# Optimization experiments

Measured on AMD Instinct MI355X. Metric: run time of the kernel, lower is better.

Reference implementation:

```python
import jax, jax.numpy as jnp
import numpy as np

L, H, W, C = 5, 32, 128, 256
HEADS, DH = 8, 32
NUM_TYPES, NUM_REL = 2, 4
INNER = HEADS * DH  # 256
LN_EPS = 1e-5


def setup_inputs() -> dict:
    key = jax.random.key(0)
    ks = jax.random.split(key, 16)
    s = 0.05
    x = jax.random.normal(ks[0], (L, H, W, C), jnp.float32)
    mask = jax.random.randint(ks[1], (H, W, 1, L), 0, 2).astype(jnp.int32)
    types = jax.random.randint(ks[2], (L,), 0, NUM_TYPES)
    # prior_encoding carries the node type in channel 2 (constant across H,W)
    prior_encoding = jnp.zeros((L, H, W, 3), jnp.float32)
    prior_encoding = prior_encoding.at[:, :, :, 2].set(
        jnp.broadcast_to(types[:, None, None].astype(jnp.float32), (L, H, W)))
    return {
        'x': x,
        'mask': mask,
        'prior_encoding': prior_encoding,
        'ln_gamma': jnp.ones((C,), jnp.float32),
        'ln_beta': jnp.zeros((C,), jnp.float32),
        'q_weight': jax.random.normal(ks[3], (NUM_TYPES, INNER, C), jnp.float32) * s,
        'q_bias': jnp.zeros((NUM_TYPES, INNER), jnp.float32),
        'k_weight': jax.random.normal(ks[4], (NUM_TYPES, INNER, C), jnp.float32) * s,
        'k_bias': jnp.zeros((NUM_TYPES, INNER), jnp.float32),
        'v_weight': jax.random.normal(ks[5], (NUM_TYPES, INNER, C), jnp.float32) * s,
        'v_bias': jnp.zeros((NUM_TYPES, INNER), jnp.float32),
        'a_weight': jax.random.normal(ks[6], (NUM_TYPES, C, INNER), jnp.float32) * s,
        'a_bias': jnp.zeros((NUM_TYPES, C), jnp.float32),
        'relation_att': jax.random.normal(ks[7], (NUM_REL, HEADS, DH, DH), jnp.float32) * s,
        'relation_msg': jax.random.normal(ks[8], (NUM_REL, HEADS, DH, DH), jnp.float32) * s,
    }


def reference(x, mask, prior_encoding, ln_gamma, ln_beta,
              q_weight, q_bias, k_weight, k_bias, v_weight, v_bias,
              a_weight, a_bias, relation_att, relation_msg):
    # --- prenorm (LayerNorm over last dim), x: (L,H,W,C) ---
    mu = jnp.mean(x, axis=-1, keepdims=True)
    var = jnp.mean(jnp.square(x - mu), axis=-1, keepdims=True)
    xn = (x - mu) * jax.lax.rsqrt(var + LN_EPS) * ln_gamma + ln_beta

    xh = jnp.transpose(xn, (1, 2, 0, 3))  # (H,W,L,C)
    types = prior_encoding[:, 0, 0, 2].astype(jnp.int32)
    types = jnp.clip(types, 0, None)  # (L,)
    n_types = q_weight.shape[0]
    heads, dh = relation_att.shape[1], relation_att.shape[2]
    Hh, Ww, Ll = xh.shape[0], xh.shape[1], xh.shape[2]

    def type_linear(w, b):  # per-token typed projection
        return jnp.einsum('hwlc,lic->hwli', xh, w[types]) + b[types]

    def to_heads(t):  # (H,W,L,inner) -> (m,H,W,L,dh)
        return jnp.transpose(t.reshape(Hh, Ww, Ll, heads, dh), (3, 0, 1, 2, 4))

    q = to_heads(type_linear(q_weight, q_bias))
    k = to_heads(type_linear(k_weight, k_bias))
    v = to_heads(type_linear(v_weight, v_bias))

    # per-edge relation matrices: rel_idx (L,L)
    rel_idx = types[:, None] * n_types + types[None, :]
    w_att = jnp.transpose(relation_att[rel_idx], (2, 0, 1, 3, 4))  # (m,L,L,dh,dh)
    w_msg = jnp.transpose(relation_msg[rel_idx], (2, 0, 1, 3, 4))  # (m,L,L,dh,dh)

    scale = jnp.asarray(dh, jnp.float32) ** -0.5
    # att_map = (q @ w_att) @ k^T, per (head, h, w, i, j)
    att = jnp.einsum('mhwip,mijpq,mhwjq->mhwij', q, w_att, k) * scale
    att = jnp.where(mask[None] == 0, jnp.float32(-1e9), att)  # mask: (1,H,W,1,L)
    att = jax.nn.softmax(att, axis=-1)

    # out = att @ (w_msg @ v)
    out = jnp.einsum('mhwij,mijpc,mhwjp->mhwic', att, w_msg, v)  # (m,H,W,L,dh)
    out = jnp.transpose(out, (1, 2, 3, 0, 4)).reshape(Hh, Ww, Ll, heads * dh)

    # typed output projection back to C
    out = jnp.einsum('hwli,lci->hwlc', out, a_weight[types]) + a_bias[types]
    return jnp.transpose(out, (2, 0, 1, 3))  # (L,H,W,C)
```

## Files before the change

kernel.cpp:

```cpp
#include <hip/hip_runtime.h>
#include <math.h>

#define LL 5
#define HH 32
#define WW 128
#define CC 256
#define HEADS 8
#define DHH 32
#define HW (HH*WW)
#define NTOK (LL*HW)
#define LN_EPS 1e-5f

typedef short bf16x8 __attribute__((ext_vector_type(8)));
typedef float f32x4 __attribute__((ext_vector_type(4)));
typedef unsigned short u16x8 __attribute__((ext_vector_type(8)));

__device__ __forceinline__ int clamp01(int t) { return t < 0 ? 0 : (t > 1 ? 1 : t); }

__device__ __forceinline__ unsigned short f2b(float f) {
    union { float f; unsigned u; } v; v.f = f;
    unsigned r = v.u + 0x7FFFu + ((v.u >> 16) & 1u);
    return (unsigned short)(r >> 16);
}
__device__ __forceinline__ float b2f(unsigned short u) {
    union { unsigned u; float f; } v; v.u = ((unsigned)u) << 16; return v.f;
}

__device__ __forceinline__ size_t frag_off(int row, int col) {
    return ((size_t)((row >> 4) * 8 + (col >> 5)) << 9)
         + (((col & 31) >> 3) << 7) + ((row & 15) << 3) + (col & 7);
}

__global__ __launch_bounds__(256) void setup_kernel(
        const float* __restrict__ x, const float* __restrict__ g, const float* __restrict__ b,
        unsigned short* __restrict__ xn,
        const float* __restrict__ qw, const float* __restrict__ aw,
        unsigned short* __restrict__ qwb, unsigned short* __restrict__ awb,
        const float* __restrict__ relA, const float* __restrict__ relM,
        const float* __restrict__ kw, const float* __restrict__ vw,
        const float* __restrict__ kb, const float* __restrict__ vb,
        unsigned short* __restrict__ wattb, unsigned short* __restrict__ wmsgb,
        float* __restrict__ batt, float* __restrict__ bmsg) {
    __shared__ float Bl[32][256];
    int blk = blockIdx.x;
    int wave = threadIdx.x >> 6, lane = threadIdx.x & 63;
    if (blk < 1280) {
        float4 gv = *(const float4*)(g + lane * 4);
        float4 bv = *(const float4*)(b + lane * 4);
        #pragma unroll
        for (int rr = 0; rr < 4; ++rr) {
            int row = blk * 16 + wave * 4 + rr;
            const float4 xv = *(const float4*)(x + (size_t)row * CC + lane * 4);
            float s1 = xv.x + xv.y + xv.z + xv.w;
            float s2 = xv.x * xv.x + xv.y * xv.y + xv.z * xv.z + xv.w * xv.w;
            #pragma unroll
            for (int off = 32; off; off >>= 1) {
                s1 += __shfl_xor(s1, off, 64);
                s2 += __shfl_xor(s2, off, 64);
            }
            float mu = s1 * (1.0f / CC);
            float inv = rsqrtf(s2 * (1.0f / CC) - mu * mu + LN_EPS);
            ushort4 o;
            o.x = f2b((xv.x - mu) * inv * gv.x + bv.x);
            o.y = f2b((xv.y - mu) * inv * gv.y + bv.y);
            o.z = f2b((xv.z - mu) * inv * gv.z + bv.z);
            o.w = f2b((xv.w - mu) * inv * gv.w + bv.w);
            *(ushort4*)(xn + frag_off(row, lane << 2)) = o;
        }
    } else if (blk < 1408) {
        int task = (blk - 1280) * 4 + wave;
        int mtx = task >> 8, rem = task & 255;
        int t = rem >> 7, panel = (rem >> 3) & 15, kk = rem & 7;
        const float* S = (mtx ? aw : qw) + (size_t)t * 65536
                       + (size_t)(panel * 16 + (lane & 15)) * 256 + kk * 32 + (lane >> 4) * 8;
        float4 f0 = *(const float4*)S;
        float4 f1 = *(const float4*)(S + 4);
        u16x8 o;
        o[0] = f2b(f0.x); o[1] = f2b(f0.y); o[2] = f2b(f0.z); o[3] = f2b(f0.w);
        o[4] = f2b(f1.x); o[5] = f2b(f1.y); o[6] = f2b(f1.z); o[7] = f2b(f1.w);
        unsigned short* D = (mtx ? awb : qwb) + (size_t)t * 65536
                          + (((size_t)(panel * 8 + kk)) << 9) + (lane << 3);
        *(u16x8*)D = o;
    } else {
        int fb = blk - 1408;
        int r = fb & 3, m = (fb >> 2) & 7, which = fb >> 5;
        int tsel = r & 1;
        const float* S  = (which ? relM : relA) + ((size_t)r * 8 + m) * 1024;
        const float* Bg = (which ? vw : kw) + (size_t)tsel * 65536 + (size_t)m * 32 * 256;
        const float* bv = (which ? vb : kb) + tsel * 256 + m * 32;
        unsigned short* Wf = (which ? wmsgb : wattb) + (size_t)r * 65536;
        float* bo = (which ? bmsg : batt) + r * 256 + m * 32;

        for (int i = threadIdx.x; i < 32 * 256; i += 256)
            Bl[i >> 8][i & 255] = Bg[(size_t)(i >> 8) * 256 + (i & 255)];
        __syncthreads();

        int a  = threadIdx.x >> 3;
        int c0 = (threadIdx.x & 7) * 4;
        float srow[32];
        #pragma unroll
        for (int bq = 0; bq < 32; ++bq)
            srow[bq] = which ? S[bq * 32 + a] : S[a * 32 + bq];
        float acc[8][4] = {{0.f}};
        #pragma unroll
        for (int bq = 0; bq < 32; ++bq) {
            float s = srow[bq];
            #pragma unroll
            for (int cc = 0; cc < 8; ++cc) {
                float4 bb = *(const float4*)&Bl[bq][c0 + cc * 32];
                acc[cc][0] += s * bb.x; acc[cc][1] += s * bb.y;
                acc[cc][2] += s * bb.z; acc[cc][3] += s * bb.w;
            }
        }
        int colpanel = m * 2 + (a >> 4);
        int jr = a & 15;
        #pragma unroll
        for (int cc = 0; cc < 8; ++cc) {
            ushort4 w4;
            w4.x = f2b(acc[cc][0]); w4.y = f2b(acc[cc][1]);
            w4.z = f2b(acc[cc][2]); w4.w = f2b(acc[cc][3]);
            *(ushort4*)(Wf + (((size_t)(colpanel * 8 + cc)) << 9)
                           + ((c0 >> 3) << 7) + (jr << 3) + (c0 & 7)) = w4;
        }
        if (threadIdx.x < 32) {
            int p = threadIdx.x;
            float s = 0.f;
            #pragma unroll
            for (int bq = 0; bq < 32; ++bq)
                s += (which ? S[bq * 32 + p] : S[p * 32 + bq]) * bv[bq];
            bo[p] = s;
        }
    }
}

__global__ __launch_bounds__(256) void gemm_qkv(const short* __restrict__ X,
        const short* __restrict__ qwb, const short* __restrict__ wattb,
        const short* __restrict__ wmsgb,
        const float* __restrict__ qb, const float* __restrict__ batt,
        const float* __restrict__ bmsg,
        const float* __restrict__ prior, unsigned short* __restrict__ OutBase) {
    __shared__ float R[4][16][68];
    int blkrow = blockIdx.x * 32;
    int s = blockIdx.y;
    int l = blkrow >> 12;
    int t = clamp01((int)prior[(size_t)l * HW * 3 + 2]);

    const short* Wp; const float* Bp;
    if (s == 0)      { Wp = qwb   + (size_t)t * 65536;                          Bp = qb   + t * 256; }
    else if (s <= 2) { int i2 = (s - 1) * 2 + t; Wp = wattb + (size_t)i2 * 65536; Bp = batt + i2 * 256; }
    else             { int i2 = (s - 3) * 2 + t; Wp = wmsgb + (size_t)i2 * 65536; Bp = bmsg + i2 * 256; }
    unsigned short* Out = OutBase + (size_t)s * NTOK * 256;

    int wave = threadIdx.x >> 6, lane = threadIdx.x & 63;
    int lr = lane & 15;
    const short* Xf = X + ((size_t)blockIdx.x << 13);

    f32x4 acc[2][4];
    #pragma unroll
    for (int mr = 0; mr < 2; ++mr)
        #pragma unroll
        for (int nr = 0; nr < 4; ++nr) acc[mr][nr] = (f32x4){0.f, 0.f, 0.f, 0.f};

    #pragma unroll
    for (int kk = 0; kk < 8; ++kk) {
        bf16x8 af[2], bf[4];
        #pragma unroll
        for (int mr = 0; mr < 2; ++mr)
            af[mr] = *(const bf16x8*)(Xf + (((size_t)(mr * 8 + kk)) << 9) + (lane << 3));
        #pragma unroll
        for (int nr = 0; nr < 4; ++nr)
            bf[nr] = *(const bf16x8*)(Wp + (((size_t)((wave * 4 + nr) * 8 + kk)) << 9) + (lane << 3));
        #pragma unroll
        for (int mr = 0; mr < 2; ++mr)
            #pragma unroll
            for (int nr = 0; nr < 4; ++nr)
                acc[mr][nr] = __builtin_amdgcn_mfma_f32_16x16x32_bf16(af[mr], bf[nr], acc[mr][nr], 0, 0, 0);
    }

    float bias[4];
    #pragma unroll
    for (int nr = 0; nr < 4; ++nr) bias[nr] = Bp[wave * 64 + nr * 16 + lr];

    int q = lane >> 4;
    int c8 = lane & 7;
    #pragma unroll
    for (int mr = 0; mr < 2; ++mr) {
        #pragma unroll
        for (int nr = 0; nr < 4; ++nr)
            #pragma unroll
            for (int rr = 0; rr < 4; ++rr)
                R[wave][q * 4 + rr][nr * 16 + lr] = acc[mr][nr][rr] + bias[nr];
        #pragma unroll
        for (int p = 0; p < 2; ++p) {
            int r = (lane >> 3) + p * 8;
            float4 v0 = *(const float4*)&R[wave][r][c8 * 8];
            float4 v1 = *(const float4*)&R[wave][r][c8 * 8 + 4];
            u16x8 w;
            w[0] = f2b(v0.x); w[1] = f2b(v0.y); w[2] = f2b(v0.z); w[3] = f2b(v0.w);
            w[4] = f2b(v1.x); w[5] = f2b(v1.y); w[6] = f2b(v1.z); w[7] = f2b(v1.w);
            *(u16x8*)(Out + (size_t)(blkrow + mr * 16 + r) * 256 + wave * 64 + c8 * 8) = w;
        }
        __builtin_amdgcn_wave_barrier();
    }
}

__global__ __launch_bounds__(256) void attn_tl(
        const unsigned short* __restrict__ QKV,
        const int* __restrict__ mask, const float* __restrict__ prior,
        unsigned short* __restrict__ attb) {
    const size_t TSTR = (size_t)NTOK * 256;
    int gid = blockIdx.x * 256 + threadIdx.x;
    int m  = gid & 7;
    int hw = (gid >> 3) & (HW - 1);
    int i  = gid >> 15;
    int t  = clamp01((int)prior[(size_t)i * HW * 3 + 2]);

    const unsigned short* Qp = QKV + (size_t)(i * HW + hw) * 256 + m * 32;
    const unsigned short* Kb = QKV + (1 + t) * TSTR + (size_t)hw * 256 + m * 32;
    const unsigned short* Vb = QKV + (3 + t) * TSTR + (size_t)hw * 256 + m * 32;

    float qf[32];
    #pragma unroll
    for (int c = 0; c < 4; ++c) {
        bf16x8 qv = *(const bf16x8*)(Qp + c * 8);
        #pragma unroll
        for (int e = 0; e < 8; ++e) qf[c * 8 + e] = b2f((unsigned short)qv[e]);
    }

    const float scale = 0.17677669529663687f;
    float s[LL];
    #pragma unroll
    for (int j = 0; j < LL; ++j) {
        const unsigned short* Kp = Kb + (size_t)j * HW * 256;
        float acc = 0.f;
        #pragma unroll
        for (int c = 0; c < 4; ++c) {
            bf16x8 kv = *(const bf16x8*)(Kp + c * 8);
            #pragma unroll
            for (int e = 0; e < 8; ++e)
                acc = fmaf(qf[c * 8 + e], b2f((unsigned short)kv[e]), acc);
        }
        int mk = mask[hw * LL + j];
        s[j] = mk ? acc * scale : -1e9f;
    }

    float mx = fmaxf(fmaxf(fmaxf(s[0], s[1]), fmaxf(s[2], s[3])), s[4]);
    float e5[LL], sum = 0.f;
    #pragma unroll
    for (int j = 0; j < LL; ++j) { e5[j] = __expf(s[j] - mx); sum += e5[j]; }
    float inv = 1.f / sum;

    float o[32];
    #pragma unroll
    for (int c = 0; c < 32; ++c) o[c] = 0.f;
    #pragma unroll
    for (int j = 0; j < LL; ++j) {
        const unsigned short* Vp = Vb + (size_t)j * HW * 256;
        float ej = e5[j];
        #pragma unroll
        for (int c = 0; c < 4; ++c) {
            bf16x8 vv = *(const bf16x8*)(Vp + c * 8);
            #pragma unroll
            for (int e = 0; e < 8; ++e)
                o[c * 8 + e] = fmaf(ej, b2f((unsigned short)vv[e]), o[c * 8 + e]);
        }
    }

    int row = i * HW + hw;
    size_t base = (((size_t)((row >> 4) * 8 + m)) << 9) + ((row & 15) << 3);
    #pragma unroll
    for (int c8 = 0; c8 < 4; ++c8) {
        u16x8 w;
        #pragma unroll
        for (int e = 0; e < 8; ++e) w[e] = f2b(o[c8 * 8 + e] * inv);
        *(u16x8*)(attb + base + c8 * 128) = w;
    }
}

__global__ __launch_bounds__(256) void gemm_a(const short* __restrict__ X,
        const short* __restrict__ W, const float* __restrict__ Bias,
        const float* __restrict__ prior, float* __restrict__ Out) {
    int blkrow = blockIdx.x * 64;
    int l = blkrow >> 12;
    int t = clamp01((int)prior[(size_t)l * HW * 3 + 2]);
    const short* Wp = W + (size_t)t * 65536;
    const float* Bp = Bias + (size_t)t * 256;

    int wave = threadIdx.x >> 6, lane = threadIdx.x & 63;
    int lr = lane & 15;
    const short* Xf = X + (((size_t)blockIdx.x * 4) << 12);

    f32x4 acc[4][4];
    #pragma unroll
    for (int mr = 0; mr < 4; ++mr)
        #pragma unroll
        for (int nr = 0; nr < 4; ++nr) acc[mr][nr] = (f32x4){0.f, 0.f, 0.f, 0.f};

    #pragma unroll
    for (int kk = 0; kk < 8; ++kk) {
        bf16x8 af[4], bf[4];
        #pragma unroll
        for (int mr = 0; mr < 4; ++mr)
            af[mr] = *(const bf16x8*)(Xf + (((size_t)(mr * 8 + kk)) << 9) + (lane << 3));
        #pragma unroll
        for (int nr = 0; nr < 4; ++nr)
            bf[nr] = *(const bf16x8*)(Wp + (((size_t)((wave * 4 + nr) * 8 + kk)) << 9) + (lane << 3));
        #pragma unroll
        for (int mr = 0; mr < 4; ++mr)
            #pragma unroll
            for (int nr = 0; nr < 4; ++nr)
                acc[mr][nr] = __builtin_amdgcn_mfma_f32_16x16x32_bf16(af[mr], bf[nr], acc[mr][nr], 0, 0, 0);
    }

    #pragma unroll
    for (int nr = 0; nr < 4; ++nr) {
        int col = wave * 64 + nr * 16 + lr;
        float bias = Bp[col];
        #pragma unroll
        for (int mr = 0; mr < 4; ++mr) {
            #pragma unroll
            for (int rr = 0; rr < 4; ++rr) {
                int row = blkrow + mr * 16 + (lane >> 4) * 4 + rr;
                Out[(size_t)row * 256 + col] = acc[mr][nr][rr] + bias;
            }
        }
    }
}

extern "C" void kernel_launch(void* const* d_in, const int* in_sizes, int n_in,
                              void* d_out, int out_size, void* d_ws, size_t ws_size,
                              hipStream_t stream) {
    (void)in_sizes; (void)n_in; (void)out_size; (void)ws_size;
    const float* x     = (const float*)d_in[0];
    const int*   mask  = (const int*)d_in[1];
    const float* prior = (const float*)d_in[2];
    const float* ln_g  = (const float*)d_in[3];
    const float* ln_b  = (const float*)d_in[4];
    const float* qw    = (const float*)d_in[5];
    const float* qb    = (const float*)d_in[6];
    const float* kw    = (const float*)d_in[7];
    const float* kb    = (const float*)d_in[8];
    const float* vw    = (const float*)d_in[9];
    const float* vb    = (const float*)d_in[10];
    const float* aw    = (const float*)d_in[11];
    const float* ab    = (const float*)d_in[12];
    const float* relA  = (const float*)d_in[13];
    const float* relM  = (const float*)d_in[14];
    float* out = (float*)d_out;

    char* ws = (char*)d_ws;
    const size_t TOKB = (size_t)NTOK * 256 * 2;
    unsigned short* xnb  = (unsigned short*)(ws);
    unsigned short* Qb   = (unsigned short*)(ws + TOKB);
    unsigned short* attb = (unsigned short*)(ws + 6 * TOKB);
    char* wsp = ws + 7 * TOKB;
    unsigned short* qwb   = (unsigned short*)(wsp);            wsp += 131072 * 2;
    unsigned short* awb   = (unsigned short*)(wsp);            wsp += 131072 * 2;
    unsigned short* wattb = (unsigned short*)(wsp);            wsp += 4 * 65536 * 2;
    unsigned short* wmsgb = (unsigned short*)(wsp);            wsp += 4 * 65536 * 2;
    float* batt = (float*)(wsp);                               wsp += 4 * 256 * 4;
    float* bmsg = (float*)(wsp);

    setup_kernel<<<1472, 256, 0, stream>>>(x, ln_g, ln_b, xnb, qw, aw, qwb, awb,
                                           relA, relM, kw, vw, kb, vb,
                                           wattb, wmsgb, batt, bmsg);

    gemm_qkv<<<dim3(NTOK / 32, 5), 256, 0, stream>>>((const short*)xnb,
            (const short*)qwb, (const short*)wattb, (const short*)wmsgb,
            qb, batt, bmsg, prior, Qb);

    attn_tl<<<(LL * HEADS * HW) / 256, 256, 0, stream>>>(Qb, mask, prior, attb);

    gemm_a<<<NTOK / 64, 256, 0, stream>>>((const short*)attb, (const short*)awb, ab, prior, out);
}
```

Before: 69.82 us.

## Fuse attention and output projection into one kernel via LDS staging

Merges the per-token attention kernel with the typed output-projection GEMM. Each block computes attention for 32 tokens × 8 heads, writes the bf16 results into shared memory in the MFMA panel layout, then runs the projection GEMM straight from LDS. This removes the global round trip of the attention buffer and one kernel launch. In exchange, the GEMM tile shrinks from 64 to 32 rows, so projection weights are reloaded twice as often and each block's GEMM waits behind a barrier.

```diff
diff --git a/kernel.cpp b/kernel.cpp
--- a/kernel.cpp
+++ b/kernel.cpp
@@ -204,109 +204,105 @@
     }
 }
 
-__global__ __launch_bounds__(256) void attn_tl(
-        const unsigned short* __restrict__ QKV,
-        const int* __restrict__ mask, const float* __restrict__ prior,
-        unsigned short* __restrict__ attb) {
+__global__ __launch_bounds__(256) void attn_proj(
+        const unsigned short* __restrict__ QKV, const short* __restrict__ awb,
+        const float* __restrict__ ab, const int* __restrict__ mask,
+        const float* __restrict__ prior, float* __restrict__ out) {
+    __shared__ unsigned short Att[32 * 256];
     const size_t TSTR = (size_t)NTOK * 256;
-    int gid = blockIdx.x * 256 + threadIdx.x;
-    int m  = gid & 7;
-    int hw = (gid >> 3) & (HW - 1);
-    int i  = gid >> 15;
-    int t  = clamp01((int)prior[(size_t)i * HW * 3 + 2]);
-
-    const unsigned short* Qp = QKV + (size_t)(i * HW + hw) * 256 + m * 32;
-    const unsigned short* Kb = QKV + (1 + t) * TSTR + (size_t)hw * 256 + m * 32;
-    const unsigned short* Vb = QKV + (3 + t) * TSTR + (size_t)hw * 256 + m * 32;
-
-    float qf[32];
-    #pragma unroll
-    for (int c = 0; c < 4; ++c) {
-        bf16x8 qv = *(const bf16x8*)(Qp + c * 8);
-        #pragma unroll
-        for (int e = 0; e < 8; ++e) qf[c * 8 + e] = b2f((unsigned short)qv[e]);
-    }
-
-    const float scale = 0.17677669529663687f;
-    float s[LL];
-    #pragma unroll
-    for (int j = 0; j < LL; ++j) {
-        const unsigned short* Kp = Kb + (size_t)j * HW * 256;
-        float acc = 0.f;
+    int tid = threadIdx.x;
+    int blkrow = blockIdx.x * 32;
+    int i = blkrow >> 12;
+    int t = clamp01((int)prior[(size_t)i * HW * 3 + 2]);
+
+    int tok = tid >> 3, m = tid & 7;
+    int row = blkrow + tok;
+    int hw = row & (HW - 1);
+
+    {
+        const unsigned short* Qp = QKV + (size_t)row * 256 + m * 32;
+        const unsigned short* Kb = QKV + (size_t)(1 + t) * TSTR + (size_t)hw * 256 + m * 32;
+        const unsigned short* Vb = QKV + (size_t)(3 + t) * TSTR + (size_t)hw * 256 + m * 32;
+
+        float qf[32];
         #pragma unroll
         for (int c = 0; c < 4; ++c) {
-            bf16x8 kv = *(const bf16x8*)(Kp + c * 8);
-            #pragma unroll
-            for (int e = 0; e < 8; ++e)
-                acc = fmaf(qf[c * 8 + e], b2f((unsigned short)kv[e]), acc);
-        }
-        int mk = mask[hw * LL + j];
-        s[j] = mk ? acc * scale : -1e9f;
-    }
-
-    float mx = fmaxf(fmaxf(fmaxf(s[0], s[1]), fmaxf(s[2], s[3])), s[4]);
-    float e5[LL], sum = 0.f;
-    #pragma unroll
-    for (int j = 0; j < LL; ++j) { e5[j] = __expf(s[j] - mx); sum += e5[j]; }
-    float inv = 1.f / sum;
-
-    float o[32];
-    #pragma unroll
-    for (int c = 0; c < 32; ++c) o[c] = 0.f;
-    #pragma unroll
-    for (int j = 0; j < LL; ++j) {
-        const unsigned short* Vp = Vb + (size_t)j * HW * 256;
-        float ej = e5[j];
-        #pragma unroll
-        for (int c = 0; c < 4; ++c) {
-            bf16x8 vv = *(const bf16x8*)(Vp + c * 8);
-            #pragma unroll
-            for (int e = 0; e < 8; ++e)
-                o[c * 8 + e] = fmaf(ej, b2f((unsigned short)vv[e]), o[c * 8 + e]);
-        }
-    }
-
-    int row = i * HW + hw;
-    size_t base = (((size_t)((row >> 4) * 8 + m)) << 9) + ((row & 15) << 3);
-    #pragma unroll
-    for (int c8 = 0; c8 < 4; ++c8) {
-        u16x8 w;
-        #pragma unroll
-        for (int e = 0; e < 8; ++e) w[e] = f2b(o[c8 * 8 + e] * inv);
-        *(u16x8*)(attb + base + c8 * 128) = w;
-    }
-}
-
-__global__ __launch_bounds__(256) void gemm_a(const short* __restrict__ X,
-        const short* __restrict__ W, const float* __restrict__ Bias,
-        const float* __restrict__ prior, float* __restrict__ Out) {
-    int blkrow = blockIdx.x * 64;
-    int l = blkrow >> 12;
-    int t = clamp01((int)prior[(size_t)l * HW * 3 + 2]);
-    const short* Wp = W + (size_t)t * 65536;
-    const float* Bp = Bias + (size_t)t * 256;
-
-    int wave = threadIdx.x >> 6, lane = threadIdx.x & 63;
-    int lr = lane & 15;
-    const short* Xf = X + (((size_t)blockIdx.x * 4) << 12);
-
-    f32x4 acc[4][4];
-    #pragma unroll
-    for (int mr = 0; mr < 4; ++mr)
+            bf16x8 qv = *(const bf16x8*)(Qp + c * 8);
+            #pragma unroll
+            for (int e = 0; e < 8; ++e) qf[c * 8 + e] = b2f((unsigned short)qv[e]);
+        }
+
+        const float scale = 0.17677669529663687f;
+        float s[LL];
+        #pragma unroll
+        for (int j = 0; j < LL; ++j) {
+            const unsigned short* Kp = Kb + (size_t)j * HW * 256;
+            float acc = 0.f;
+            #pragma unroll
+            for (int c = 0; c < 4; ++c) {
+                bf16x8 kv = *(const bf16x8*)(Kp + c * 8);
+                #pragma unroll
+                for (int e = 0; e < 8; ++e)
+                    acc = fmaf(qf[c * 8 + e], b2f((unsigned short)kv[e]), acc);
+            }
+            int mk = mask[hw * LL + j];
+            s[j] = mk ? acc * scale : -1e9f;
+        }
+
+        float mx = fmaxf(fmaxf(fmaxf(s[0], s[1]), fmaxf(s[2], s[3])), s[4]);
+        float e5[LL], sum = 0.f;
+        #pragma unroll
+        for (int j = 0; j < LL; ++j) { e5[j] = __expf(s[j] - mx); sum += e5[j]; }
+        float inv = 1.f / sum;
+
+        float o[32];
+        #pragma unroll
+        for (int c = 0; c < 32; ++c) o[c] = 0.f;
+        #pragma unroll
+        for (int j = 0; j < LL; ++j) {
+            const unsigned short* Vp = Vb + (size_t)j * HW * 256;
+            float ej = e5[j];
+            #pragma unroll
+            for (int c = 0; c < 4; ++c) {
+                bf16x8 vv = *(const bf16x8*)(Vp + c * 8);
+                #pragma unroll
+                for (int e = 0; e < 8; ++e)
+                    o[c * 8 + e] = fmaf(ej, b2f((unsigned short)vv[e]), o[c * 8 + e]);
+            }
+        }
+
+        int panel = tok >> 4, tr = tok & 15;
+        #pragma unroll
+        for (int c8 = 0; c8 < 4; ++c8) {
+            u16x8 w;
+            #pragma unroll
+            for (int e = 0; e < 8; ++e) w[e] = f2b(o[c8 * 8 + e] * inv);
+            *(u16x8*)(&Att[((panel * 8 + m) << 9) + c8 * 128 + tr * 8]) = w;
+        }
+    }
+    __syncthreads();
+
+    int wave = tid >> 6, lane = tid & 63, lr = lane & 15;
+    const short* Wp = awb + (size_t)t * 65536;
+    const float* Bp = ab + (size_t)t * 256;
+
+    f32x4 acc[2][4];
+    #pragma unroll
+    for (int mr = 0; mr < 2; ++mr)
         #pragma unroll
         for (int nr = 0; nr < 4; ++nr) acc[mr][nr] = (f32x4){0.f, 0.f, 0.f, 0.f};
 
     #pragma unroll
     for (int kk = 0; kk < 8; ++kk) {
-        bf16x8 af[4], bf[4];
-        #pragma unroll
-        for (int mr = 0; mr < 4; ++mr)
-            af[mr] = *(const bf16x8*)(Xf + (((size_t)(mr * 8 + kk)) << 9) + (lane << 3));
+        bf16x8 af[2], bf[4];
+        #pragma unroll
+        for (int mr = 0; mr < 2; ++mr)
+            af[mr] = *(const bf16x8*)((const short*)Att + ((mr * 8 + kk) << 9) + (lane << 3));
         #pragma unroll
         for (int nr = 0; nr < 4; ++nr)
             bf[nr] = *(const bf16x8*)(Wp + (((size_t)((wave * 4 + nr) * 8 + kk)) << 9) + (lane << 3));
         #pragma unroll
-        for (int mr = 0; mr < 4; ++mr)
+        for (int mr = 0; mr < 2; ++mr)
             #pragma unroll
             for (int nr = 0; nr < 4; ++nr)
                 acc[mr][nr] = __builtin_amdgcn_mfma_f32_16x16x32_bf16(af[mr], bf[nr], acc[mr][nr], 0, 0, 0);
@@ -317,11 +313,11 @@
         int col = wave * 64 + nr * 16 + lr;
         float bias = Bp[col];
         #pragma unroll
-        for (int mr = 0; mr < 4; ++mr) {
+        for (int mr = 0; mr < 2; ++mr) {
             #pragma unroll
             for (int rr = 0; rr < 4; ++rr) {
-                int row = blkrow + mr * 16 + (lane >> 4) * 4 + rr;
-                Out[(size_t)row * 256 + col] = acc[mr][nr][rr] + bias;
+                int orow = blkrow + mr * 16 + (lane >> 4) * 4 + rr;
+                out[(size_t)orow * 256 + col] = acc[mr][nr][rr] + bias;
             }
         }
     }
@@ -352,8 +348,7 @@
     const size_t TOKB = (size_t)NTOK * 256 * 2;
     unsigned short* xnb  = (unsigned short*)(ws);
     unsigned short* Qb   = (unsigned short*)(ws + TOKB);
-    unsigned short* attb = (unsigned short*)(ws + 6 * TOKB);
-    char* wsp = ws + 7 * TOKB;
+    char* wsp = ws + 6 * TOKB;
     unsigned short* qwb   = (unsigned short*)(wsp);            wsp += 131072 * 2;
     unsigned short* awb   = (unsigned short*)(wsp);            wsp += 131072 * 2;
     unsigned short* wattb = (unsigned short*)(wsp);            wsp += 4 * 65536 * 2;
@@ -369,7 +364,5 @@
             (const short*)qwb, (const short*)wattb, (const short*)wmsgb,
             qb, batt, bmsg, prior, Qb);
 
-    attn_tl<<<(LL * HEADS * HW) / 256, 256, 0, stream>>>(Qb, mask, prior, attb);
-
-    gemm_a<<<NTOK / 64, 256, 0, stream>>>((const short*)attb, (const short*)awb, ab, prior, out);
-}
+    attn_proj<<<NTOK / 32, 256, 0, stream>>>(Qb, (const short*)awb, ab, mask, prior, out);
+}
```

New measurement: 64.49 us, median of 2. -7.6%, faster.
